# Kernel optimization log

Measured on AMD Instinct MI355X. Metric: run time of the kernel, lower is better.

The kernel has to match this reference:

```python
import jax, jax.numpy as jnp
import numpy as np

B, S, H, T, W = 8, 512, 768, 4, 10
NEG = -1e9

def _u(key, shape, k):
    return jax.random.uniform(key, shape, jnp.float32, -k, k)

def setup_inputs():
    key = jax.random.key(0)
    ks = jax.random.split(key, 20)
    kh = float(1.0 / np.sqrt(H)); kt = float(1.0 / np.sqrt(T))
    return dict(
        embeddings=jax.random.normal(ks[0], (B, S, H), jnp.float32),
        l1f_wih=_u(ks[1], (4 * H, H), kh), l1f_whh=_u(ks[2], (4 * H, H), kh), l1f_b=_u(ks[3], (4 * H,), kh),
        l1r_wih=_u(ks[4], (4 * H, H), kh), l1r_whh=_u(ks[5], (4 * H, H), kh), l1r_b=_u(ks[6], (4 * H,), kh),
        attn_w=_u(ks[7], (3 * H,), kh), attn_b=_u(ks[8], (1,), kh),
        l2f_wih=_u(ks[9], (4 * T, 2 * H), kt), l2f_whh=_u(ks[10], (4 * T, T), kt), l2f_b=_u(ks[11], (4 * T,), kt),
        l2r_wih=_u(ks[12], (4 * T, 2 * H), kt), l2r_whh=_u(ks[13], (4 * T, T), kt), l2r_b=_u(ks[14], (4 * T,), kt),
        crf_start=0.1 * jax.random.normal(ks[15], (T,), jnp.float32),
        crf_end=0.1 * jax.random.normal(ks[16], (T,), jnp.float32),
        crf_trans=0.1 * jax.random.normal(ks[17], (T, T), jnp.float32),
        window_size=W,
    )

def _lstm_dir(x, w_ih, w_hh, b):
    # x: [B,S,D] -> [B,S,Hh]; torch gate order i,f,g,o
    Hh = w_hh.shape[1]
    bs = x.shape[0]
    xs = (jnp.einsum('bsd,gd->bsg', x, w_ih) + b).transpose(1, 0, 2)  # [S,B,4Hh]
    def step(carry, xt):
        h, c = carry
        g = xt + h @ w_hh.T
        i, f, gg, o = jnp.split(g, 4, axis=-1)
        c = jax.nn.sigmoid(f) * c + jax.nn.sigmoid(i) * jnp.tanh(gg)
        h = jax.nn.sigmoid(o) * jnp.tanh(c)
        return (h, c), h
    init = (jnp.zeros((bs, Hh), x.dtype), jnp.zeros((bs, Hh), x.dtype))
    _, hs = jax.lax.scan(step, init, xs)
    return hs.transpose(1, 0, 2)

def _bilstm(x, pf, pr):
    hf = _lstm_dir(x, *pf)
    hr = _lstm_dir(x[:, ::-1], *pr)[:, ::-1]
    return jnp.concatenate([hf, hr], axis=-1)

def _win_attn(h, w, b, win):
    # h: [B,S,D]; similarity(hi,hj) = w1.hi + w2.hj + w3.(hi*hj) + b
    bs, s, d = h.shape
    w1, w2, w3 = w[:d], w[d:2 * d], w[2 * d:]
    offs = jnp.arange(-win, win + 1)                      # [K]
    idx = jnp.arange(s)[:, None] + offs[None, :]          # [S,K]
    valid = (idx >= 0) & (idx < s)
    idxc = jnp.clip(idx, 0, s - 1)
    hw = h[:, idxc]                                       # [B,S,K,D]
    scores = (h @ w1)[:, :, None] \
        + jnp.einsum('bskd,d->bsk', hw, w2) \
        + jnp.einsum('bsd,bskd->bsk', h * w3, hw) + b[0]
    scores = jnp.where(valid[None], scores, NEG)
    aw = jax.nn.softmax(scores, axis=-1)                  # [B,S,K]
    return jnp.einsum('bsk,bskd->bsd', aw, hw)

def _viterbi(em, start, end, trans):
    # em: [B,S,T] -> tags [B,S]
    score0 = start[None] + em[:, 0]
    ems = em.transpose(1, 0, 2)[1:]                       # [S-1,B,T]
    def step(score, e_t):
        nxt = score[:, :, None] + trans[None]             # [B,Tprev,T]
        best = jnp.max(nxt, axis=1) + e_t
        bp = jnp.argmax(nxt, axis=1)
        return best, bp
    final, bps = jax.lax.scan(step, score0, ems)          # bps [S-1,B,T]
    final = final + end[None]
    last = jnp.argmax(final, axis=-1)                     # [B]
    def back(tag, bp):
        prev = jnp.take_along_axis(bp, tag[:, None], axis=1)[:, 0]
        return prev, prev
    _, tags_rev = jax.lax.scan(back, last, bps[::-1])
    return jnp.concatenate([tags_rev[::-1], last[None]], axis=0).transpose(1, 0)

def reference(embeddings, l1f_wih, l1f_whh, l1f_b, l1r_wih, l1r_whh, l1r_b,
              attn_w, attn_b, l2f_wih, l2f_whh, l2f_b, l2r_wih, l2r_whh, l2r_b,
              crf_start, crf_end, crf_trans, window_size):
    h1 = _bilstm(embeddings, (l1f_wih, l1f_whh, l1f_b), (l1r_wih, l1r_whh, l1r_b))
    d = h1.shape[-1] // 2
    hs = h1[..., :d] + h1[..., d:]                        # sum of directions [B,S,H]
    att = _win_attn(hs, attn_w, attn_b, int(window_size))
    x2 = jnp.concatenate([hs, att], axis=-1)              # [B,S,2H]
    h2 = _bilstm(x2, (l2f_wih, l2f_whh, l2f_b), (l2r_wih, l2r_whh, l2r_b))
    d2 = h2.shape[-1] // 2
    em = h2[..., :d2] + h2[..., d2:]                      # CRF emissions [B,S,T]
    tags = _viterbi(em, crf_start, crf_end, crf_trans)
    return tags, em
```

## Files before the change

kernel.cpp:

```cpp
#include <hip/hip_runtime.h>
#include <math.h>

#define SEQ 512
#define BATCH 8
#define HID 768
#define G4 3072
#define CHUNK 128
#define NEGV (-1000000000.0f)

typedef float v4f __attribute__((ext_vector_type(4)));
typedef float v2f __attribute__((ext_vector_type(2)));

__device__ __forceinline__ float sigm(float x) { return 1.0f / (1.0f + expf(-x)); }

__device__ __forceinline__ v2f fma2(v2f a, v2f b, v2f c) {
#if __has_builtin(__builtin_elementwise_fma)
  return __builtin_elementwise_fma(a, b, c);
#else
  v2f r; r.x = __builtin_fmaf(a.x, b.x, c.x); r.y = __builtin_fmaf(a.y, b.y, c.y);
  return r;
#endif
}

__device__ __forceinline__ float wred(float x) {
#pragma unroll
  for (int off = 32; off > 0; off >>= 1) x += __shfl_xor(x, off, 64);
  return x;
}

__device__ __forceinline__ void load2_f4_sc(const float* p0, const float* p1,
                                            v4f& a, v4f& b) {
  asm volatile("global_load_dwordx4 %0, %2, off sc0 sc1\n\t"
               "global_load_dwordx4 %1, %3, off sc0 sc1\n\t"
               "s_waitcnt vmcnt(0)"
               : "=&v"(a), "=&v"(b) : "v"(p0), "v"(p1) : "memory");
}
__device__ __forceinline__ int load_i_sc(const int* p) {
  int r;
  asm volatile("global_load_dword %0, %1, off sc0 sc1\n\ts_waitcnt vmcnt(0)"
               : "=v"(r) : "v"(p) : "memory");
  return r;
}
__device__ __forceinline__ void store_f_sc(float* p, float v) {
  asm volatile("global_store_dword %0, %1, off sc0 sc1" :: "v"(p), "v"(v) : "memory");
}
__device__ __forceinline__ void store_i_sc(int* p, int v) {
  asm volatile("global_store_dword %0, %1, off sc0 sc1" :: "v"(p), "v"(v) : "memory");
}

template <int CTRL, int RMASK>
__device__ __forceinline__ float dpp_add(float x) {
  int y = __builtin_amdgcn_update_dpp(0, __float_as_int(x), CTRL, RMASK, 0xF, false);
  return x + __int_as_float(y);
}
__device__ __forceinline__ float reduce32(float x) {
  x = dpp_add<0x121, 0xF>(x);
  x = dpp_add<0x122, 0xF>(x);
  x = dpp_add<0x124, 0xF>(x);
  x = dpp_add<0x128, 0xF>(x);
  x = dpp_add<0x142, 0xA>(x);
  return x;
}

__global__ void k_init(float* __restrict__ hbuf, int* __restrict__ flags) {
  int i = blockIdx.x * blockDim.x + threadIdx.x;
  if (i < 2 * 2 * BATCH * HID) hbuf[i] = 0.0f;
  if (i < 4096) flags[i] = 0;
}

__global__ __launch_bounds__(256) void k_proj1(
    const float* __restrict__ emb,
    const float* __restrict__ w_f, const float* __restrict__ b_f,
    const float* __restrict__ w_r, const float* __restrict__ b_r,
    float* __restrict__ xs_f, float* __restrict__ xs_r, int chunk) {
  __shared__ float As[16][132];
  __shared__ float Bs[16][132];
  const int tid = threadIdx.x;
  const int bn0 = blockIdx.x * 128;
  const int bb  = blockIdx.y;
  const int dir = blockIdx.z;
  const float* W    = dir ? w_r : w_f;
  const float* bias = dir ? b_r : b_f;
  float* xs = dir ? xs_r : xs_f;

  v2f acc2[8][4];
#pragma unroll
  for (int i = 0; i < 8; i++)
#pragma unroll
    for (int j = 0; j < 4; j++) acc2[i][j] = (v2f){0.0f, 0.0f};

  const int mload = tid & 127;
  const int kq0   = tid >> 7;
  const int tglob = dir ? (SEQ - 1 - (chunk * CHUNK + mload)) : (chunk * CHUNK + mload);
  const float* arow = emb + (size_t)(bb * SEQ + tglob) * HID;
  const float* brow = W + (size_t)(bn0 + mload) * HID;
  const int tm = tid & 15, tn = tid >> 4;

  const float* aptr = arow + kq0 * 4;
  const float* bptr = brow + kq0 * 4;
  const int rA = kq0 * 4;
  const int rB = (kq0 + 2) * 4;

  float4 a0 = *(const float4*)(aptr);
  float4 a1 = *(const float4*)(aptr + 8);
  float4 b0 = *(const float4*)(bptr);
  float4 b1 = *(const float4*)(bptr + 8);

  for (int kt = 0; kt < HID; kt += 16) {
    As[rA + 0][mload] = a0.x; As[rA + 1][mload] = a0.y;
    As[rA + 2][mload] = a0.z; As[rA + 3][mload] = a0.w;
    As[rB + 0][mload] = a1.x; As[rB + 1][mload] = a1.y;
    As[rB + 2][mload] = a1.z; As[rB + 3][mload] = a1.w;
    Bs[rA + 0][mload] = b0.x; Bs[rA + 1][mload] = b0.y;
    Bs[rA + 2][mload] = b0.z; Bs[rA + 3][mload] = b0.w;
    Bs[rB + 0][mload] = b1.x; Bs[rB + 1][mload] = b1.y;
    Bs[rB + 2][mload] = b1.z; Bs[rB + 3][mload] = b1.w;
    __syncthreads();
    if (kt + 16 < HID) {
      a0 = *(const float4*)(aptr + kt + 16);
      a1 = *(const float4*)(aptr + kt + 24);
      b0 = *(const float4*)(bptr + kt + 16);
      b1 = *(const float4*)(bptr + kt + 24);
    }
#pragma unroll
    for (int k = 0; k < 16; k++) {
      float4 c0 = *(const float4*)&As[k][tm * 8];
      float4 c1 = *(const float4*)&As[k][tm * 8 + 4];
      float4 d0 = *(const float4*)&Bs[k][tn * 8];
      float4 d1 = *(const float4*)&Bs[k][tn * 8 + 4];
      float av[8] = {c0.x, c0.y, c0.z, c0.w, c1.x, c1.y, c1.z, c1.w};
      v2f bv2[4] = {{d0.x, d0.y}, {d0.z, d0.w}, {d1.x, d1.y}, {d1.z, d1.w}};
#pragma unroll
      for (int i = 0; i < 8; i++) {
        v2f avv = {av[i], av[i]};
#pragma unroll
        for (int jj = 0; jj < 4; jj++) acc2[i][jj] = fma2(avv, bv2[jj], acc2[i][jj]);
      }
    }
    __syncthreads();
  }
#pragma unroll
  for (int i = 0; i < 8; i++) {
    int row = tm * 8 + i;
    size_t base = (size_t)(bb * CHUNK + row) * G4 + bn0 + tn * 8;
#pragma unroll
    for (int jj = 0; jj < 4; jj++) {
      xs[base + 2 * jj]     = acc2[i][jj].x + bias[bn0 + tn * 8 + 2 * jj];
      xs[base + 2 * jj + 1] = acc2[i][jj].y + bias[bn0 + tn * 8 + 2 * jj + 1];
    }
  }
}

__global__ __launch_bounds__(384, 2) void k_rec1(
    const float* __restrict__ whh_f, const float* __restrict__ whh_r,
    const float* __restrict__ xs_f, const float* __restrict__ xs_r,
    float* __restrict__ hbuf, float* __restrict__ cbuf, int* __restrict__ flags,
    float* __restrict__ hf, float* __restrict__ hr, int t0, int init) {
  __shared__ float hlds[4 * HID];
  const int tid = threadIdx.x;
  const int bid = blockIdx.x;
  const int dir = bid >> 7;
  const int bh  = (bid >> 6) & 1;
  const int jb  = bid & 63;
  const int J0  = jb * 12;
  const int grp = dir * 2 + bh;
  const int g  = tid >> 5;
  const int kq = tid & 31;
  const int j  = J0 + g;

  const float* W  = dir ? whh_r : whh_f;
  const float* xs = dir ? xs_r  : xs_f;
  float* harr = dir ? hr : hf;

  float wreg[4][24];
#pragma unroll
  for (int gate = 0; gate < 4; gate++) {
#pragma unroll
    for (int q = 0; q < 6; q++) {
      *(v4f*)&wreg[gate][q * 4] =
          *(const v4f*)&W[(size_t)(gate * HID + j) * HID + q * 128 + kq * 4];
    }
  }

  float cc[4];
#pragma unroll
  for (int b = 0; b < 4; b++) cc[b] = 0.0f;
  if (!init && kq == 16) {
#pragma unroll
    for (int b = 0; b < 4; b++) cc[b] = cbuf[bid * 48 + g * 4 + b];
  }

  for (int stp = 0; stp < CHUNK; stp++) {
    const int s = t0 + stp;
    const int par = s & 1;

    float xsv[4][4];
    if (kq == 16) {
#pragma unroll
      for (int b = 0; b < 4; b++) {
        const size_t xbase = (size_t)((bh * 4 + b) * CHUNK + stp) * G4 + j;
#pragma unroll
        for (int gate = 0; gate < 4; gate++)
          xsv[b][gate] = xs[xbase + gate * HID];
      }
    }

    if (tid < 64) {
      const int* fp = flags + (grp * 64 + tid) * 16;
      while (load_i_sc(fp) < s) { __builtin_amdgcn_s_sleep(4); }
    }
    __syncthreads();

    {
      const float* src = hbuf + (size_t)((par * 2 + dir) * BATCH + bh * 4) * HID + tid * 8;
      v4f a, b4;
      load2_f4_sc(src, src + 4, a, b4);
      *(v4f*)&hlds[tid * 8]     = a;
      *(v4f*)&hlds[tid * 8 + 4] = b4;
    }
    __syncthreads();

    float acc[4][4];
#pragma unroll
    for (int gate = 0; gate < 4; gate++)
#pragma unroll
      for (int b = 0; b < 4; b++) acc[gate][b] = 0.0f;
#pragma unroll
    for (int b = 0; b < 4; b++) {
      float hk[24];
#pragma unroll
      for (int q = 0; q < 6; q++)
        *(v4f*)&hk[q * 4] = *(const v4f*)&hlds[b * HID + q * 128 + kq * 4];
#pragma unroll
      for (int gate = 0; gate < 4; gate++)
#pragma unroll
        for (int k = 0; k < 24; k++) acc[gate][b] += wreg[gate][k] * hk[k];
    }
#pragma unroll
    for (int gate = 0; gate < 4; gate++)
#pragma unroll
      for (int b = 0; b < 4; b++) acc[gate][b] = reduce32(acc[gate][b]);

    float hv[4];
    int t = 0;
    if (kq == 16) {
      t = dir ? (SEQ - 1 - s) : s;
#pragma unroll
      for (int b = 0; b < 4; b++) {
        const int bg = bh * 4 + b;
        float iv = acc[0][b] + xsv[b][0];
        float fv = acc[1][b] + xsv[b][1];
        float gv = acc[2][b] + xsv[b][2];
        float ov = acc[3][b] + xsv[b][3];
        cc[b] = sigm(fv) * cc[b] + sigm(iv) * tanhf(gv);
        hv[b] = sigm(ov) * tanhf(cc[b]);
        store_f_sc(hbuf + (size_t)(((par ^ 1) * 2 + dir) * BATCH + bg) * HID + j, hv[b]);
      }
    }
    asm volatile("s_waitcnt vmcnt(0)" ::: "memory");
    __syncthreads();
    if (tid == 0) store_i_sc(flags + (grp * 64 + jb) * 16, s + 1);
    if (kq == 16) {
#pragma unroll
      for (int b = 0; b < 4; b++)
        harr[(size_t)((bh * 4 + b) * SEQ + t) * HID + j] = hv[b];
    }
  }
  if (kq == 16) {
#pragma unroll
    for (int b = 0; b < 4; b++) cbuf[bid * 48 + g * 4 + b] = cc[b];
  }
}

__global__ void k_sum(float* __restrict__ hf, const float* __restrict__ hr) {
  int i = blockIdx.x * 256 + threadIdx.x;
  float4 a = ((const float4*)hf)[i];
  float4 b = ((const float4*)hr)[i];
  a.x += b.x; a.y += b.y; a.z += b.z; a.w += b.w;
  ((float4*)hf)[i] = a;
}

__global__ __launch_bounds__(64) void k_attn(
    const float* __restrict__ hs, const float* __restrict__ attn_w,
    const float* __restrict__ attn_b, float* __restrict__ att) {
  const int l = threadIdx.x;
  const int s = blockIdx.x, b = blockIdx.y;
  const float* hrow = hs + (size_t)(b * SEQ + s) * HID;
  float v[12];
  float u1p = 0.0f;
#pragma unroll
  for (int jj = 0; jj < 12; jj++) {
    int d = l + 64 * jj;
    float x = hrow[d];
    u1p += x * attn_w[d];
    v[jj] = attn_w[HID + d] + x * attn_w[2 * HID + d];
  }
  float u1 = wred(u1p) + attn_b[0];
  float sc[21];
  for (int o = 0; o < 21; o++) {
    int s2 = s + o - 10;
    if (s2 >= 0 && s2 < SEQ) {
      const float* h2 = hs + (size_t)(b * SEQ + s2) * HID;
      float p = 0.0f;
#pragma unroll
      for (int jj = 0; jj < 12; jj++) p += h2[l + 64 * jj] * v[jj];
      sc[o] = wred(p) + u1;
    } else {
      sc[o] = NEGV;
    }
  }
  float m = sc[0];
#pragma unroll
  for (int o = 1; o < 21; o++) m = fmaxf(m, sc[o]);
  float sum = 0.0f;
#pragma unroll
  for (int o = 0; o < 21; o++) { sc[o] = expf(sc[o] - m); sum += sc[o]; }
  float inv = 1.0f / sum;
  float acc[12];
#pragma unroll
  for (int jj = 0; jj < 12; jj++) acc[jj] = 0.0f;
  for (int o = 0; o < 21; o++) {
    int s2 = s + o - 10;
    if (s2 < 0 || s2 >= SEQ) continue;
    float a = sc[o] * inv;
    const float* h2 = hs + (size_t)(b * SEQ + s2) * HID;
#pragma unroll
    for (int jj = 0; jj < 12; jj++) acc[jj] += a * h2[l + 64 * jj];
  }
  float* orow = att + (size_t)(b * SEQ + s) * HID;
#pragma unroll
  for (int jj = 0; jj < 12; jj++) orow[l + 64 * jj] = acc[jj];
}

__global__ __launch_bounds__(256) void k_proj2(
    const float* __restrict__ hs, const float* __restrict__ att,
    const float* __restrict__ w2f, const float* __restrict__ b2f,
    const float* __restrict__ w2r, const float* __restrict__ b2r,
    float* __restrict__ xs2) {
  __shared__ __align__(16) float x2[2 * HID];
  __shared__ float part[32][9];
  const int tid = threadIdx.x;
  const int s = blockIdx.x, b = blockIdx.y;
  size_t base = (size_t)(b * SEQ + s) * HID;
  for (int i = tid; i < 2 * HID; i += 256)
    x2[i] = (i < HID) ? hs[base + i] : att[base + i - HID];
  __syncthreads();
  const int gid = tid & 31, pp = tid >> 5;
  const int d = gid >> 4, g = gid & 15;
  const float4* w4 = (const float4*)((d ? w2r : w2f) + (size_t)g * (2 * HID));
  const float4* x4 = (const float4*)x2;
  float p = 0.0f;
  for (int e = pp * 48; e < pp * 48 + 48; e++) {
    float4 xv = x4[e];
    float4 wv = w4[e];
    p += xv.x * wv.x + xv.y * wv.y + xv.z * wv.z + xv.w * wv.w;
  }
  part[gid][pp] = p;
  __syncthreads();
  if (tid < 32) {
    float sumv = (d ? b2r : b2f)[g];
#pragma unroll
    for (int q = 0; q < 8; q++) sumv += part[gid][q];
    xs2[(size_t)((d * BATCH + b) * SEQ + s) * 16 + g] = sumv;
  }
}

__global__ __launch_bounds__(256) void k_rec2(
    const float* __restrict__ xs2,
    const float* __restrict__ whh_f, const float* __restrict__ whh_r,
    float* __restrict__ h2) {
  const int tid = threadIdx.x;
  const int lane = tid & 63;
  const int hb = (tid >> 6) * 4 + (lane >> 4);
  const int g = lane & 15;
  const int d = hb >> 3;
  const int base = lane & 48;
  const float* whh = (d ? whh_r : whh_f) + g * 4;
  const float w0 = whh[0], w1 = whh[1], w2 = whh[2], w3 = whh[3];
  const float* xrow = xs2 + (size_t)hb * SEQ * 16 + g;
  float c = 0.0f, h = 0.0f;
  float xv = xrow[(d ? (SEQ - 1) : 0) * 16];
  for (int st = 0; st < SEQ; st++) {
    const int t = d ? (SEQ - 1 - st) : st;
    const int tn = d ? (SEQ - 2 - st) : (st + 1);
    float xnext = (st + 1 < SEQ) ? xrow[tn * 16] : 0.0f;
    float h0 = __shfl(h, base + 0, 64);
    float h1 = __shfl(h, base + 1, 64);
    float h2v = __shfl(h, base + 2, 64);
    float h3 = __shfl(h, base + 3, 64);
    float gv = xv + w0 * h0 + w1 * h1 + w2 * h2v + w3 * h3;
    const int jj = g & 3;
    float iv = __shfl(gv, base + jj, 64);
    float fv = __shfl(gv, base + 4 + jj, 64);
    float gq = __shfl(gv, base + 8 + jj, 64);
    float ov = __shfl(gv, base + 12 + jj, 64);
    c = sigm(fv) * c + sigm(iv) * tanhf(gq);
    h = sigm(ov) * tanhf(c);
    if (g < 4) h2[((size_t)hb * SEQ + t) * 4 + g] = h;
    xv = xnext;
  }
}

__global__ void k_em(const float* __restrict__ h2, float* __restrict__ out) {
  int i = blockIdx.x * 256 + threadIdx.x;
  if (i < BATCH * SEQ * 4) out[BATCH * SEQ + i] = h2[i] + h2[BATCH * SEQ * 4 + i];
}

__global__ __launch_bounds__(32) void k_viterbi(
    float* __restrict__ out, const float* __restrict__ start,
    const float* __restrict__ endw, const float* __restrict__ trans) {
  __shared__ unsigned char bp[SEQ - 1][32];
  const int l = threadIdx.x;
  const int b = l >> 2, j = l & 3;
  const float* em = out + BATCH * SEQ;
  const float tr0 = trans[0 * 4 + j], tr1 = trans[1 * 4 + j];
  const float tr2 = trans[2 * 4 + j], tr3 = trans[3 * 4 + j];
  float score = start[j] + em[((size_t)b * SEQ + 0) * 4 + j];
  for (int t = 1; t < SEQ; t++) {
    float s0 = __shfl(score, b * 4 + 0, 64);
    float s1 = __shfl(score, b * 4 + 1, 64);
    float s2 = __shfl(score, b * 4 + 2, 64);
    float s3 = __shfl(score, b * 4 + 3, 64);
    float v0 = s0 + tr0, v1 = s1 + tr1, v2 = s2 + tr2, v3 = s3 + tr3;
    float best = v0; int arg = 0;
    if (v1 > best) { best = v1; arg = 1; }
    if (v2 > best) { best = v2; arg = 2; }
    if (v3 > best) { best = v3; arg = 3; }
    bp[t - 1][l] = (unsigned char)arg;
    score = best + em[((size_t)b * SEQ + t) * 4 + j];
  }
  score += endw[j];
  float f0 = __shfl(score, b * 4 + 0, 64);
  float f1 = __shfl(score, b * 4 + 1, 64);
  float f2 = __shfl(score, b * 4 + 2, 64);
  float f3 = __shfl(score, b * 4 + 3, 64);
  if (j == 0) {
    float bbv = f0; int last = 0;
    if (f1 > bbv) { bbv = f1; last = 1; }
    if (f2 > bbv) { bbv = f2; last = 2; }
    if (f3 > bbv) { bbv = f3; last = 3; }
    int tag = last;
    out[b * SEQ + (SEQ - 1)] = (float)tag;
    for (int t = SEQ - 2; t >= 0; t--) {
      tag = bp[t][b * 4 + tag];
      out[b * SEQ + t] = (float)tag;
    }
  }
}

extern "C" void kernel_launch(void* const* d_in, const int* in_sizes, int n_in,
                              void* d_out, int out_size, void* d_ws, size_t ws_size,
                              hipStream_t stream) {
  const float* emb      = (const float*)d_in[0];
  const float* l1f_wih  = (const float*)d_in[1];
  const float* l1f_whh  = (const float*)d_in[2];
  const float* l1f_b    = (const float*)d_in[3];
  const float* l1r_wih  = (const float*)d_in[4];
  const float* l1r_whh  = (const float*)d_in[5];
  const float* l1r_b    = (const float*)d_in[6];
  const float* attn_w   = (const float*)d_in[7];
  const float* attn_b   = (const float*)d_in[8];
  const float* l2f_wih  = (const float*)d_in[9];
  const float* l2f_whh  = (const float*)d_in[10];
  const float* l2f_b    = (const float*)d_in[11];
  const float* l2r_wih  = (const float*)d_in[12];
  const float* l2r_whh  = (const float*)d_in[13];
  const float* l2r_b    = (const float*)d_in[14];
  const float* crf_start= (const float*)d_in[15];
  const float* crf_end  = (const float*)d_in[16];
  const float* crf_trans= (const float*)d_in[17];

  float* ws = (float*)d_ws;
  const size_t NCH = (size_t)BATCH * CHUNK * G4;
  float* xs_f = ws;
  float* xs_r = xs_f + NCH;
  float* hf   = xs_r + NCH;
  float* hr   = hf + (size_t)BATCH * SEQ * HID;
  float* hbuf = hr + (size_t)BATCH * SEQ * HID;
  float* cbuf = hbuf + 2 * 2 * BATCH * HID;
  float* h2   = cbuf + 256 * 48;
  int*   flags= (int*)(h2 + 2 * BATCH * SEQ * 4);
  float* xs2  = xs_f;
  float* att  = xs_r;
  float* hs   = hf;

  k_init<<<dim3(96), dim3(256), 0, stream>>>(hbuf, flags);

  for (int c = 0; c < 4; c++) {
    k_proj1<<<dim3(24, 8, 2), dim3(256), 0, stream>>>(
        emb, l1f_wih, l1f_b, l1r_wih, l1r_b, xs_f, xs_r, c);
    k_rec1<<<dim3(256), dim3(384), 0, stream>>>(
        l1f_whh, l1r_whh, xs_f, xs_r, hbuf, cbuf, flags, hf, hr,
        c * CHUNK, c == 0 ? 1 : 0);
  }

  k_sum<<<dim3(3072), dim3(256), 0, stream>>>(hf, hr);
  k_attn<<<dim3(SEQ, BATCH), dim3(64), 0, stream>>>(hs, attn_w, attn_b, att);
  k_proj2<<<dim3(SEQ, BATCH), dim3(256), 0, stream>>>(
      hs, att, l2f_wih, l2f_b, l2r_wih, l2r_b, xs2);
  k_rec2<<<dim3(1), dim3(256), 0, stream>>>(xs2, l2f_whh, l2r_whh, h2);
  k_em<<<dim3(64), dim3(256), 0, stream>>>(h2, (float*)d_out);
  k_viterbi<<<dim3(1), dim3(32), 0, stream>>>((float*)d_out, crf_start, crf_end, crf_trans);
}
```

Baseline: 3.696 ms.

## Halve recurrent LSTM block count with 768-thread blocks and pad GEMM LDS tiles

```diff
diff --git a/kernel.cpp b/kernel.cpp
--- a/kernel.cpp
+++ b/kernel.cpp
@@ -28,12 +28,11 @@
   return x;
 }
 
-__device__ __forceinline__ void load2_f4_sc(const float* p0, const float* p1,
-                                            v4f& a, v4f& b) {
-  asm volatile("global_load_dwordx4 %0, %2, off sc0 sc1\n\t"
-               "global_load_dwordx4 %1, %3, off sc0 sc1\n\t"
-               "s_waitcnt vmcnt(0)"
-               : "=&v"(a), "=&v"(b) : "v"(p0), "v"(p1) : "memory");
+__device__ __forceinline__ v4f load_f4_sc(const float* p) {
+  v4f a;
+  asm volatile("global_load_dwordx4 %0, %1, off sc0 sc1\n\ts_waitcnt vmcnt(0)"
+               : "=v"(a) : "v"(p) : "memory");
+  return a;
 }
 __device__ __forceinline__ int load_i_sc(const int* p) {
   int r;
@@ -68,13 +67,14 @@
   if (i < 4096) flags[i] = 0;
 }
 
+#define CMAP(c) ((c) + (((c) >> 5) << 2))
 __global__ __launch_bounds__(256) void k_proj1(
     const float* __restrict__ emb,
     const float* __restrict__ w_f, const float* __restrict__ b_f,
     const float* __restrict__ w_r, const float* __restrict__ b_r,
     float* __restrict__ xs_f, float* __restrict__ xs_r, int chunk) {
-  __shared__ float As[16][132];
-  __shared__ float Bs[16][132];
+  __shared__ float As[16][144];
+  __shared__ float Bs[16][144];
   const int tid = threadIdx.x;
   const int bn0 = blockIdx.x * 128;
   const int bb  = blockIdx.y;
@@ -95,6 +95,9 @@
   const float* arow = emb + (size_t)(bb * SEQ + tglob) * HID;
   const float* brow = W + (size_t)(bn0 + mload) * HID;
   const int tm = tid & 15, tn = tid >> 4;
+  const int cw = CMAP(mload);
+  const int cA = CMAP(tm * 8);
+  const int cB = CMAP(tn * 8);
 
   const float* aptr = arow + kq0 * 4;
   const float* bptr = brow + kq0 * 4;
@@ -107,14 +110,14 @@
   float4 b1 = *(const float4*)(bptr + 8);
 
   for (int kt = 0; kt < HID; kt += 16) {
-    As[rA + 0][mload] = a0.x; As[rA + 1][mload] = a0.y;
-    As[rA + 2][mload] = a0.z; As[rA + 3][mload] = a0.w;
-    As[rB + 0][mload] = a1.x; As[rB + 1][mload] = a1.y;
-    As[rB + 2][mload] = a1.z; As[rB + 3][mload] = a1.w;
-    Bs[rA + 0][mload] = b0.x; Bs[rA + 1][mload] = b0.y;
-    Bs[rA + 2][mload] = b0.z; Bs[rA + 3][mload] = b0.w;
-    Bs[rB + 0][mload] = b1.x; Bs[rB + 1][mload] = b1.y;
-    Bs[rB + 2][mload] = b1.z; Bs[rB + 3][mload] = b1.w;
+    As[rA + 0][cw] = a0.x; As[rA + 1][cw] = a0.y;
+    As[rA + 2][cw] = a0.z; As[rA + 3][cw] = a0.w;
+    As[rB + 0][cw] = a1.x; As[rB + 1][cw] = a1.y;
+    As[rB + 2][cw] = a1.z; As[rB + 3][cw] = a1.w;
+    Bs[rA + 0][cw] = b0.x; Bs[rA + 1][cw] = b0.y;
+    Bs[rA + 2][cw] = b0.z; Bs[rA + 3][cw] = b0.w;
+    Bs[rB + 0][cw] = b1.x; Bs[rB + 1][cw] = b1.y;
+    Bs[rB + 2][cw] = b1.z; Bs[rB + 3][cw] = b1.w;
     __syncthreads();
     if (kt + 16 < HID) {
       a0 = *(const float4*)(aptr + kt + 16);
@@ -124,10 +127,10 @@
     }
 #pragma unroll
     for (int k = 0; k < 16; k++) {
-      float4 c0 = *(const float4*)&As[k][tm * 8];
-      float4 c1 = *(const float4*)&As[k][tm * 8 + 4];
-      float4 d0 = *(const float4*)&Bs[k][tn * 8];
-      float4 d1 = *(const float4*)&Bs[k][tn * 8 + 4];
+      float4 c0 = *(const float4*)&As[k][cA];
+      float4 c1 = *(const float4*)&As[k][cA + 4];
+      float4 d0 = *(const float4*)&Bs[k][cB];
+      float4 d1 = *(const float4*)&Bs[k][cB + 4];
       float av[8] = {c0.x, c0.y, c0.z, c0.w, c1.x, c1.y, c1.z, c1.w};
       v2f bv2[4] = {{d0.x, d0.y}, {d0.z, d0.w}, {d1.x, d1.y}, {d1.z, d1.w}};
 #pragma unroll
@@ -151,7 +154,7 @@
   }
 }
 
-__global__ __launch_bounds__(384, 2) void k_rec1(
+__global__ __launch_bounds__(768, 1) void k_rec1(
     const float* __restrict__ whh_f, const float* __restrict__ whh_r,
     const float* __restrict__ xs_f, const float* __restrict__ xs_r,
     float* __restrict__ hbuf, float* __restrict__ cbuf, int* __restrict__ flags,
@@ -159,10 +162,10 @@
   __shared__ float hlds[4 * HID];
   const int tid = threadIdx.x;
   const int bid = blockIdx.x;
-  const int dir = bid >> 7;
-  const int bh  = (bid >> 6) & 1;
-  const int jb  = bid & 63;
-  const int J0  = jb * 12;
+  const int dir = bid >> 6;
+  const int bh  = (bid >> 5) & 1;
+  const int jb  = bid & 31;
+  const int J0  = jb * 24;
   const int grp = dir * 2 + bh;
   const int g  = tid >> 5;
   const int kq = tid & 31;
@@ -187,7 +190,7 @@
   for (int b = 0; b < 4; b++) cc[b] = 0.0f;
   if (!init && kq == 16) {
 #pragma unroll
-    for (int b = 0; b < 4; b++) cc[b] = cbuf[bid * 48 + g * 4 + b];
+    for (int b = 0; b < 4; b++) cc[b] = cbuf[bid * 96 + g * 4 + b];
   }
 
   for (int stp = 0; stp < CHUNK; stp++) {
@@ -205,18 +208,15 @@
       }
     }
 
-    if (tid < 64) {
-      const int* fp = flags + (grp * 64 + tid) * 16;
+    if (tid < 32) {
+      const int* fp = flags + (grp * 32 + tid) * 16;
       while (load_i_sc(fp) < s) { __builtin_amdgcn_s_sleep(4); }
     }
     __syncthreads();
 
     {
-      const float* src = hbuf + (size_t)((par * 2 + dir) * BATCH + bh * 4) * HID + tid * 8;
-      v4f a, b4;
-      load2_f4_sc(src, src + 4, a, b4);
-      *(v4f*)&hlds[tid * 8]     = a;
-      *(v4f*)&hlds[tid * 8 + 4] = b4;
+      const float* src = hbuf + (size_t)((par * 2 + dir) * BATCH + bh * 4) * HID + tid * 4;
+      *(v4f*)&hlds[tid * 4] = load_f4_sc(src);
     }
     __syncthreads();
 
@@ -259,7 +259,7 @@
     }
     asm volatile("s_waitcnt vmcnt(0)" ::: "memory");
     __syncthreads();
-    if (tid == 0) store_i_sc(flags + (grp * 64 + jb) * 16, s + 1);
+    if (tid == 0) store_i_sc(flags + (grp * 32 + jb) * 16, s + 1);
     if (kq == 16) {
 #pragma unroll
       for (int b = 0; b < 4; b++)
@@ -268,7 +268,7 @@
   }
   if (kq == 16) {
 #pragma unroll
-    for (int b = 0; b < 4; b++) cbuf[bid * 48 + g * 4 + b] = cc[b];
+    for (int b = 0; b < 4; b++) cbuf[bid * 96 + g * 4 + b] = cc[b];
   }
 }
 
@@ -489,7 +489,7 @@
   for (int c = 0; c < 4; c++) {
     k_proj1<<<dim3(24, 8, 2), dim3(256), 0, stream>>>(
         emb, l1f_wih, l1f_b, l1r_wih, l1r_b, xs_f, xs_r, c);
-    k_rec1<<<dim3(256), dim3(384), 0, stream>>>(
+    k_rec1<<<dim3(128), dim3(768), 0, stream>>>(
         l1f_whh, l1r_whh, xs_f, xs_r, hbuf, cbuf, flags, hf, hr,
         c * CHUNK, c == 0 ? 1 : 0);
   }
```

After: 4.964 ms. 34.3% more time.
